# Kernel tuning notes

Measured on AMD Instinct MI355X. Metric: run time of the kernel, lower is better.

Reference implementation:

```python
import jax, jax.numpy as jnp
import numpy as np

N_NODES = 50000


def _gin_aggregate(x, src, dst):
    # sum_{j in N(i)} x_j via scatter-add over edges; eps=0 so add self term
    msg = x[src]  # [E, d]
    return x + jax.ops.segment_sum(msg, dst, num_segments=N_NODES)


def _mlp(h, Wa, ba, Wb, bb):
    return jax.nn.relu(h @ Wa + ba) @ Wb + bb


def setup_inputs() -> dict:
    key = jax.random.key(0)
    ks = jax.random.split(key, 12)
    d_in, d_h, n_cls, n_edges = 128, 128, 40, 800000
    x = jax.random.normal(ks[0], (N_NODES, d_in), dtype=jnp.float32)
    edge_index = jax.random.randint(ks[1], (2, n_edges), 0, N_NODES, dtype=jnp.int64)
    s = lambda k, sh: jax.random.normal(k, sh, dtype=jnp.float32) / np.sqrt(sh[0])
    return {
        "x": x,
        "edge_index": edge_index,
        "W11": s(ks[2], (d_in, 2 * d_h)), "b11": jnp.zeros((2 * d_h,), jnp.float32),
        "W12": s(ks[3], (2 * d_h, d_h)), "b12": jnp.zeros((d_h,), jnp.float32),
        "W21": s(ks[4], (d_h, 2 * d_h)), "b21": jnp.zeros((2 * d_h,), jnp.float32),
        "W22": s(ks[5], (2 * d_h, d_h)), "b22": jnp.zeros((d_h,), jnp.float32),
        "Wfc": s(ks[6], (d_h, n_cls)), "bfc": jnp.zeros((n_cls,), jnp.float32),
    }


def reference(x, edge_index, W11, b11, W12, b12, W21, b21, W22, b22, Wfc, bfc):
    src, dst = edge_index[0], edge_index[1]
    # GINConv 1: aggregate then MLP, followed by ReLU
    h = _mlp(_gin_aggregate(x, src, dst), W11, b11, W12, b12)
    h = jax.nn.relu(h)
    # GINConv 2
    h = _mlp(_gin_aggregate(h, src, dst), W21, b21, W22, b22)
    h = jax.nn.relu(h)
    # final classifier
    return h @ Wfc + bfc
```

## Files before the change

kernel.cpp:

```cpp
#include <hip/hip_runtime.h>

#define N_NODES 50000
#define N_EDGES 800000
#define NBUCK   392
#define EPB     2048
#define NSB     391
#define CAPB    2560

typedef __attribute__((ext_vector_type(8))) short short8;
typedef __attribute__((ext_vector_type(4))) float floatx4;

__device__ __forceinline__ float ubits(unsigned int b) {
    union { unsigned int i; float f; } v;
    v.i = b;
    return v.f;
}
__device__ __forceinline__ unsigned short f2b(float f) {
    union { float f; unsigned int i; } v;
    v.f = f;
    unsigned int r = v.i + 0x7FFFu + ((v.i >> 16) & 1u);
    return (unsigned short)(r >> 16);
}

__device__ __forceinline__ void pack_s1(const float* __restrict__ W,
                                        unsigned short* __restrict__ Wp,
                                        int blk, int tid) {
    int p = blk * 256 + tid;
    int j = p & 7, t2 = (p >> 3) & 255, v = p >> 11;
    int w = t2 >> 6, lane = t2 & 63, quad = lane >> 4, qm = lane & 15;
    int c = v >> 3, ks = (v >> 1) & 3, nt = v & 1;
    int k = ks * 32 + quad * 8 + j;
    int n = c * 128 + w * 32 + nt * 16 + qm;
    Wp[p] = f2b(W[k * 256 + n]);
}
__device__ __forceinline__ void pack_s2(const float* __restrict__ W,
                                        unsigned short* __restrict__ Wp,
                                        int blk, int tid) {
    int p = blk * 256 + tid;
    int j = p & 7, t2 = (p >> 3) & 255, v2 = p >> 11;
    int w = t2 >> 6, lane = t2 & 63, quad = lane >> 4, qm = lane & 15;
    int c2 = v2 >> 3, ks = v2 & 7;
    int k = ks * 32 + quad * 8 + j;
    int n = c2 * 32 + (w >> 1) * 16 + qm;
    Wp[p] = f2b(W[k * 128 + n]);
}

__global__ __launch_bounds__(256) void hist_conv(
    const int* __restrict__ dstv, const float* __restrict__ x,
    int* __restrict__ cnt, unsigned short* __restrict__ xb) {
    const int bid = blockIdx.x;
    const int tid = threadIdx.x;
    if (bid < NSB) {
        __shared__ int hist[NBUCK];
        const int k = bid;
        const int e0 = k * EPB;
        for (int i = tid; i < NBUCK; i += 256) hist[i] = 0;
        __syncthreads();
#pragma unroll
        for (int j = 0; j < EPB / 256; ++j) {
            int e = e0 + j * 256 + tid;
            if (e < N_EDGES) atomicAdd(&hist[dstv[e] >> 7], 1);
        }
        __syncthreads();
        for (int i = tid; i < NBUCK; i += 256) cnt[i * NSB + k] = hist[i];
    } else {
        int i = (bid - NSB) * 256 + tid;
        const float4 a = *reinterpret_cast<const float4*>(x + (size_t)i * 8);
        const float4 b = *reinterpret_cast<const float4*>(x + (size_t)i * 8 + 4);
        ushort4 u0, u1;
        u0.x = f2b(a.x); u0.y = f2b(a.y); u0.z = f2b(a.z); u0.w = f2b(a.w);
        u1.x = f2b(b.x); u1.y = f2b(b.y); u1.z = f2b(b.z); u1.w = f2b(b.w);
        *reinterpret_cast<ushort4*>(xb + (size_t)i * 8) = u0;
        *reinterpret_cast<ushort4*>(xb + (size_t)i * 8 + 4) = u1;
    }
}

__global__ __launch_bounds__(256) void scan_conv(
    const int* __restrict__ cnt, int* __restrict__ sbase,
    const float* __restrict__ W11, const float* __restrict__ W12,
    const float* __restrict__ W21, const float* __restrict__ W22,
    const float* __restrict__ Wfc,
    unsigned short* __restrict__ Wp11, unsigned short* __restrict__ Wp12,
    unsigned short* __restrict__ Wp21, unsigned short* __restrict__ Wp22,
    unsigned short* __restrict__ Wfct) {
    const int bid = blockIdx.x;
    const int tid = threadIdx.x;
    if (bid < NBUCK) {
        __shared__ int ps[256];
        __shared__ int sc[512];
        const int b = bid;
        sc[tid] = (tid < NSB) ? cnt[b * NSB + tid] : 0;
        sc[tid + 256] = (tid + 256 < NSB) ? cnt[b * NSB + tid + 256] : 0;
        __syncthreads();
        const int c0 = sc[2 * tid], c1 = sc[2 * tid + 1];
        ps[tid] = c0 + c1;
        __syncthreads();
        for (int off = 1; off < 256; off <<= 1) {
            int u = (tid >= off) ? ps[tid - off] : 0;
            __syncthreads();
            ps[tid] += u;
            __syncthreads();
        }
        if (tid < 196) {
            const int off0 = ps[tid] - (c0 + c1);
            sbase[b * 392 + 2 * tid] = off0;
            sbase[b * 392 + 2 * tid + 1] = off0 + c0;
        }
    } else if (bid < NBUCK + 128) {
        pack_s1(W11, Wp11, bid - NBUCK, tid);
    } else if (bid < NBUCK + 384) {
        pack_s2(W12, Wp12, bid - NBUCK - 128, tid);
    } else if (bid < NBUCK + 512) {
        pack_s1(W21, Wp21, bid - NBUCK - 384, tid);
    } else if (bid < NBUCK + 768) {
        pack_s2(W22, Wp22, bid - NBUCK - 512, tid);
    } else {
        int idx = (bid - NBUCK - 768) * 256 + tid;
        int n = idx >> 7, k = idx & 127;
        Wfct[idx] = (n < 40) ? f2b(Wfc[k * 40 + n]) : (unsigned short)0;
    }
}

__global__ __launch_bounds__(256) void place_compact(
    const int* __restrict__ srcv, const int* __restrict__ dstv,
    const int* __restrict__ sbase, int* __restrict__ bufc) {
    __shared__ int cur[NBUCK];
    const int k = blockIdx.x;
    const int tid = threadIdx.x;
    for (int i = tid; i < NBUCK; i += 256) cur[i] = sbase[i * 392 + k];
    __syncthreads();
    const int e0 = k * EPB;
#pragma unroll
    for (int j = 0; j < EPB / 256; ++j) {
        int e = e0 + j * 256 + tid;
        if (e < N_EDGES) {
            int d = dstv[e];
            int b = d >> 7;
            int pos = atomicAdd(&cur[b], 1);
            bufc[b * CAPB + pos] = srcv[e] | ((d & 127) << 16);
        }
    }
}

__global__ __launch_bounds__(256) void finish_buckets(
    const int* __restrict__ sbase, const int* __restrict__ bufc,
    int* __restrict__ e_src, int* __restrict__ row_ptr) {
    __shared__ int nc[128];
    __shared__ int ps[128];
    const int b = blockIdx.x;
    const int tid = threadIdx.x;
    const int S = sbase[b * 392 + 391];
    const int gb = b * CAPB;
    if (tid < 128) nc[tid] = 0;
    __syncthreads();
    for (int t = tid; t < S; t += 256)
        atomicAdd(&nc[(bufc[gb + t] >> 16) & 127], 1);
    __syncthreads();
    if (tid < 128) ps[tid] = nc[tid];
    __syncthreads();
    for (int off = 1; off < 128; off <<= 1) {
        int u = (tid >= off && tid < 128) ? ps[tid - off] : 0;
        __syncthreads();
        if (tid < 128) ps[tid] += u;
        __syncthreads();
    }
    if (tid < 128) {
        const int excl = ps[tid] - nc[tid];
        row_ptr[b * 129 + tid] = gb + excl;
        nc[tid] = gb + excl;
    }
    if (tid == 0) row_ptr[b * 129 + 128] = gb + S;
    __syncthreads();
    for (int t = tid; t < S; t += 256) {
        int p = bufc[gb + t];
        int pos = atomicAdd(&nc[(p >> 16) & 127], 1);
        e_src[pos] = p & 0xFFFF;
    }
}

__global__ __launch_bounds__(256) void agg_bf16q(const unsigned short* __restrict__ X,
                                                 const int* __restrict__ row_ptr,
                                                 const int* __restrict__ e_src,
                                                 unsigned short* __restrict__ agg) {
    const int node = (blockIdx.x * 256 + threadIdx.x) >> 6;
    const int lane = threadIdx.x & 63;
    const int qw = lane >> 4, ql = lane & 15;
    const size_t off = (size_t)ql * 8;

    const int rp = node + (node >> 7);
    const int beg = row_ptr[rp], end = row_ptr[rp + 1];
    float acc[8];
#pragma unroll
    for (int k = 0; k < 8; ++k) acc[k] = 0.f;

    if (qw == 0) {
        uint4 u = *reinterpret_cast<const uint4*>(X + (size_t)node * 128 + off);
        const unsigned int* up = (const unsigned int*)&u;
#pragma unroll
        for (int k = 0; k < 4; ++k) {
            acc[2 * k]     += ubits(up[k] << 16);
            acc[2 * k + 1] += ubits(up[k] & 0xFFFF0000u);
        }
    }

    int e = beg + qw;
    for (; e + 12 < end; e += 16) {
        const int s0 = e_src[e], s1 = e_src[e + 4], s2 = e_src[e + 8], s3 = e_src[e + 12];
        uint4 u0 = *reinterpret_cast<const uint4*>(X + (size_t)s0 * 128 + off);
        uint4 u1 = *reinterpret_cast<const uint4*>(X + (size_t)s1 * 128 + off);
        uint4 u2 = *reinterpret_cast<const uint4*>(X + (size_t)s2 * 128 + off);
        uint4 u3 = *reinterpret_cast<const uint4*>(X + (size_t)s3 * 128 + off);
        const unsigned int* p0 = (const unsigned int*)&u0;
        const unsigned int* p1 = (const unsigned int*)&u1;
        const unsigned int* p2 = (const unsigned int*)&u2;
        const unsigned int* p3 = (const unsigned int*)&u3;
#pragma unroll
        for (int k = 0; k < 4; ++k) {
            acc[2 * k]     += ubits(p0[k] << 16) + ubits(p1[k] << 16)
                            + ubits(p2[k] << 16) + ubits(p3[k] << 16);
            acc[2 * k + 1] += ubits(p0[k] & 0xFFFF0000u) + ubits(p1[k] & 0xFFFF0000u)
                            + ubits(p2[k] & 0xFFFF0000u) + ubits(p3[k] & 0xFFFF0000u);
        }
    }
    for (; e + 4 < end; e += 8) {
        const int s0 = e_src[e], s1 = e_src[e + 4];
        uint4 u0 = *reinterpret_cast<const uint4*>(X + (size_t)s0 * 128 + off);
        uint4 u1 = *reinterpret_cast<const uint4*>(X + (size_t)s1 * 128 + off);
        const unsigned int* p0 = (const unsigned int*)&u0;
        const unsigned int* p1 = (const unsigned int*)&u1;
#pragma unroll
        for (int k = 0; k < 4; ++k) {
            acc[2 * k]     += ubits(p0[k] << 16) + ubits(p1[k] << 16);
            acc[2 * k + 1] += ubits(p0[k] & 0xFFFF0000u) + ubits(p1[k] & 0xFFFF0000u);
        }
    }
    if (e < end) {
        const int s = e_src[e];
        uint4 u = *reinterpret_cast<const uint4*>(X + (size_t)s * 128 + off);
        const unsigned int* p = (const unsigned int*)&u;
#pragma unroll
        for (int k = 0; k < 4; ++k) {
            acc[2 * k]     += ubits(p[k] << 16);
            acc[2 * k + 1] += ubits(p[k] & 0xFFFF0000u);
        }
    }

#pragma unroll
    for (int k = 0; k < 8; ++k) acc[k] += __shfl_xor(acc[k], 32);
#pragma unroll
    for (int k = 0; k < 8; ++k) acc[k] += __shfl_xor(acc[k], 16);

    if (qw == 0) {
        ushort4 o0, o1;
        o0.x = f2b(acc[0]); o0.y = f2b(acc[1]); o0.z = f2b(acc[2]); o0.w = f2b(acc[3]);
        o1.x = f2b(acc[4]); o1.y = f2b(acc[5]); o1.z = f2b(acc[6]); o1.w = f2b(acc[7]);
        unsigned short* p = agg + (size_t)node * 128 + off;
        *reinterpret_cast<ushort4*>(p) = o0;
        *reinterpret_cast<ushort4*>(p + 4) = o1;
    }
}

template <bool FUSE>
__global__ __launch_bounds__(256, 2) void mlp_fused(
    const unsigned short* __restrict__ X, const unsigned short* __restrict__ Wp1,
    const float* __restrict__ b1, const unsigned short* __restrict__ Wp2,
    const float* __restrict__ b2, unsigned short* __restrict__ Y,
    const unsigned short* __restrict__ Wfct, const float* __restrict__ bfc,
    float* __restrict__ out, int M) {
    __shared__ __align__(16) char smem[FUSE ? 68608 : 51200];
    unsigned short* A  = (unsigned short*)smem;
    unsigned short* T  = (unsigned short*)(smem + 17408);
    unsigned short* Hf = (unsigned short*)(smem + 51200);

    const int tid = threadIdx.x;
    const int m0 = blockIdx.x * 64;
    const int lane = tid & 63, w = tid >> 6;
    const int qm = lane & 15, quad = lane >> 4;

    short8 wb1[16];
#pragma unroll
    for (int v = 0; v < 16; ++v)
        wb1[v] = *reinterpret_cast<const short8*>(Wp1 + ((v * 256 + tid) << 3));

#pragma unroll
    for (int j = 0; j < 4; ++j) {
        int i = j * 256 + tid;
        int r = i >> 4, c8 = (i & 15) << 3;
        uint4 v = {0, 0, 0, 0};
        if (m0 + r < M) v = *reinterpret_cast<const uint4*>(X + (size_t)(m0 + r) * 128 + c8);
        *reinterpret_cast<uint4*>(&A[r * 136 + c8]) = v;
    }
    __syncthreads();

#pragma unroll
    for (int c = 0; c < 2; ++c) {
        floatx4 acc1[4][2];
#pragma unroll
        for (int mt = 0; mt < 4; ++mt)
#pragma unroll
            for (int nt = 0; nt < 2; ++nt) acc1[mt][nt] = {0.f, 0.f, 0.f, 0.f};
#pragma unroll
        for (int ks = 0; ks < 4; ++ks) {
            const int kb = ks * 32 + quad * 8;
            short8 a[4];
#pragma unroll
            for (int mt = 0; mt < 4; ++mt)
                a[mt] = *reinterpret_cast<const short8*>(&A[(mt * 16 + qm) * 136 + kb]);
#pragma unroll
            for (int mt = 0; mt < 4; ++mt)
#pragma unroll
                for (int nt = 0; nt < 2; ++nt)
                    acc1[mt][nt] = __builtin_amdgcn_mfma_f32_16x16x32_bf16(
                        a[mt], wb1[c * 8 + ks * 2 + nt], acc1[mt][nt], 0, 0, 0);
        }
#pragma unroll
        for (int nt = 0; nt < 2; ++nt) {
            const int jcol = c * 128 + w * 32 + nt * 16 + qm;
            const float bj = b1[jcol];
#pragma unroll
            for (int mt = 0; mt < 4; ++mt)
#pragma unroll
                for (int r = 0; r < 4; ++r)
                    T[(mt * 16 + quad * 4 + r) * 264 + jcol] =
                        f2b(fmaxf(acc1[mt][nt][r] + bj, 0.f));
        }
    }

    short8 wb2[32];
#pragma unroll
    for (int v = 0; v < 32; ++v)
        wb2[v] = *reinterpret_cast<const short8*>(Wp2 + ((v * 256 + tid) << 3));
    __syncthreads();

#pragma unroll
    for (int c2 = 0; c2 < 4; ++c2) {
        floatx4 acc2[2];
        acc2[0] = {0.f, 0.f, 0.f, 0.f};
        acc2[1] = {0.f, 0.f, 0.f, 0.f};
#pragma unroll
        for (int ks = 0; ks < 8; ++ks) {
            const int kb = ks * 32 + quad * 8;
            short8 t0 = *reinterpret_cast<const short8*>(&T[((w & 1) * 32 + qm) * 264 + kb]);
            short8 t1 = *reinterpret_cast<const short8*>(&T[((w & 1) * 32 + 16 + qm) * 264 + kb]);
            acc2[0] = __builtin_amdgcn_mfma_f32_16x16x32_bf16(t0, wb2[c2 * 8 + ks], acc2[0], 0, 0, 0);
            acc2[1] = __builtin_amdgcn_mfma_f32_16x16x32_bf16(t1, wb2[c2 * 8 + ks], acc2[1], 0, 0, 0);
        }

        const int ncol = c2 * 32 + (w >> 1) * 16 + qm;
        const float bj = b2[ncol];
        if (!FUSE) {
#pragma unroll
            for (int mt2 = 0; mt2 < 2; ++mt2)
#pragma unroll
                for (int r = 0; r < 4; ++r) {
                    int row = m0 + (w & 1) * 32 + mt2 * 16 + quad * 4 + r;
                    if (row < M)
                        Y[(size_t)row * 128 + ncol] = f2b(fmaxf(acc2[mt2][r] + bj, 0.f));
                }
        } else {
#pragma unroll
            for (int mt2 = 0; mt2 < 2; ++mt2)
#pragma unroll
                for (int r = 0; r < 4; ++r)
                    Hf[((w & 1) * 32 + mt2 * 16 + quad * 4 + r) * 136 + ncol] =
                        f2b(fmaxf(acc2[mt2][r] + bj, 0.f));
        }
    }

    if (FUSE) {
        __syncthreads();
        floatx4 cacc[3];
#pragma unroll
        for (int nt = 0; nt < 3; ++nt) cacc[nt] = {0.f, 0.f, 0.f, 0.f};
#pragma unroll
        for (int c2 = 0; c2 < 4; ++c2) {
            short8 hf = *reinterpret_cast<const short8*>(
                &Hf[(w * 16 + qm) * 136 + c2 * 32 + quad * 8]);
#pragma unroll
            for (int nt = 0; nt < 3; ++nt) {
                short8 bf = *reinterpret_cast<const short8*>(
                    Wfct + (nt * 16 + qm) * 128 + c2 * 32 + quad * 8);
                cacc[nt] = __builtin_amdgcn_mfma_f32_16x16x32_bf16(hf, bf, cacc[nt], 0, 0, 0);
            }
        }
#pragma unroll
        for (int nt = 0; nt < 3; ++nt) {
            int col = nt * 16 + qm;
            if (col < 40) {
                const float bj = bfc[col];
#pragma unroll
                for (int r = 0; r < 4; ++r) {
                    int row = m0 + w * 16 + quad * 4 + r;
                    if (row < M) out[(size_t)row * 40 + col] = cacc[nt][r] + bj;
                }
            }
        }
    }
}

extern "C" void kernel_launch(void* const* d_in, const int* in_sizes, int n_in,
                              void* d_out, int out_size, void* d_ws, size_t ws_size,
                              hipStream_t stream) {
    const float* x   = (const float*)d_in[0];
    const int*   ei  = (const int*)d_in[1];
    const float* W11 = (const float*)d_in[2];
    const float* b11 = (const float*)d_in[3];
    const float* W12 = (const float*)d_in[4];
    const float* b12 = (const float*)d_in[5];
    const float* W21 = (const float*)d_in[6];
    const float* b21 = (const float*)d_in[7];
    const float* W22 = (const float*)d_in[8];
    const float* b22 = (const float*)d_in[9];
    const float* Wfc = (const float*)d_in[10];
    const float* bfc = (const float*)d_in[11];
    float* out = (float*)d_out;

    const int* srcv = ei;
    const int* dstv = ei + N_EDGES;

    unsigned short* agg  = (unsigned short*)d_ws;
    unsigned short* h    = agg + (size_t)N_NODES * 128;
    unsigned short* xb   = h   + (size_t)N_NODES * 128;
    unsigned short* Wp11 = xb  + (size_t)N_NODES * 128;
    unsigned short* Wp12 = Wp11 + 32768;
    unsigned short* Wp21 = Wp12 + 65536;
    unsigned short* Wp22 = Wp21 + 32768;
    unsigned short* Wfct = Wp22 + 65536;
    int* cnt     = (int*)(Wfct + 48 * 128);
    int* sbase   = cnt + 153664;
    int* row_ptr = sbase + 153664;
    int* e_src   = row_ptr + 50688;
    int* bufc    = e_src + (size_t)NBUCK * CAPB;

    hist_conv<<<NSB + 3125, 256, 0, stream>>>(dstv, x, cnt, xb);

    scan_conv<<<NBUCK + 792, 256, 0, stream>>>(
        cnt, sbase, W11, W12, W21, W22, Wfc,
        Wp11, Wp12, Wp21, Wp22, Wfct);

    place_compact<<<NSB, 256, 0, stream>>>(srcv, dstv, sbase, bufc);

    finish_buckets<<<NBUCK, 256, 0, stream>>>(sbase, bufc, e_src, row_ptr);

    const int agg_blocks = N_NODES * 64 / 256;
    const int mlp_blocks = (N_NODES + 63) / 64;

    agg_bf16q<<<agg_blocks, 256, 0, stream>>>(xb, row_ptr, e_src, agg);
    mlp_fused<false><<<mlp_blocks, 256, 0, stream>>>(
        agg, Wp11, b11, Wp12, b12, h, nullptr, nullptr, nullptr, N_NODES);
    agg_bf16q<<<agg_blocks, 256, 0, stream>>>(h, row_ptr, e_src, agg);
    mlp_fused<true><<<mlp_blocks, 256, 0, stream>>>(
        agg, Wp21, b21, Wp22, b22, nullptr, Wfct, bfc, out, N_NODES);
}
```

Before: 226.1 us.

## Replace histogram-scan-place pipeline with global atomic bucket reservation

The separate histogram, per-bucket scan and placement kernels are merged into one scatter kernel. Each block reserves its slots in every bucket with a global atomicAdd on a per-bucket counter, then writes edges into them. The per-bucket CSR finish now runs inside the weight-conversion kernel. This drops two launches and the large count and base arrays, at the cost of a memset, global atomic contention, and edge order within a bucket that varies from run to run (float summation order may change).

Result: no change. 223.8 us (-1.0%).

```diff
diff --git a/kernel.cpp b/kernel.cpp
--- a/kernel.cpp
+++ b/kernel.cpp
@@ -45,24 +45,44 @@
     Wp[p] = f2b(W[k * 128 + n]);
 }
 
-__global__ __launch_bounds__(256) void hist_conv(
-    const int* __restrict__ dstv, const float* __restrict__ x,
-    int* __restrict__ cnt, unsigned short* __restrict__ xb) {
+__global__ __launch_bounds__(256) void scatter_all(
+    const int* __restrict__ srcv, const int* __restrict__ dstv,
+    const float* __restrict__ x,
+    int* __restrict__ bcount, int* __restrict__ bufc,
+    unsigned short* __restrict__ xb) {
     const int bid = blockIdx.x;
     const int tid = threadIdx.x;
     if (bid < NSB) {
         __shared__ int hist[NBUCK];
-        const int k = bid;
-        const int e0 = k * EPB;
+        __shared__ int base[NBUCK];
+        const int e0 = bid * EPB;
+        int d[8], s[8];
+#pragma unroll
+        for (int j = 0; j < 8; ++j) {
+            int e = e0 + j * 256 + tid;
+            if (e < N_EDGES) { d[j] = dstv[e]; s[j] = srcv[e]; }
+            else d[j] = -1;
+        }
         for (int i = tid; i < NBUCK; i += 256) hist[i] = 0;
         __syncthreads();
 #pragma unroll
-        for (int j = 0; j < EPB / 256; ++j) {
-            int e = e0 + j * 256 + tid;
-            if (e < N_EDGES) atomicAdd(&hist[dstv[e] >> 7], 1);
-        }
-        __syncthreads();
-        for (int i = tid; i < NBUCK; i += 256) cnt[i * NSB + k] = hist[i];
+        for (int j = 0; j < 8; ++j)
+            if (d[j] >= 0) atomicAdd(&hist[d[j] >> 7], 1);
+        __syncthreads();
+        for (int i = tid; i < NBUCK; i += 256) {
+            int c = hist[i];
+            base[i] = c ? atomicAdd(&bcount[i], c) : 0;
+            hist[i] = 0;
+        }
+        __syncthreads();
+#pragma unroll
+        for (int j = 0; j < 8; ++j) {
+            if (d[j] >= 0) {
+                int b = d[j] >> 7;
+                int r = atomicAdd(&hist[b], 1);
+                bufc[b * CAPB + base[b] + r] = s[j] | ((d[j] & 127) << 16);
+            }
+        }
     } else {
         int i = (bid - NSB) * 256 + tid;
         const float4 a = *reinterpret_cast<const float4*>(x + (size_t)i * 8);
@@ -75,8 +95,9 @@
     }
 }
 
-__global__ __launch_bounds__(256) void scan_conv(
-    const int* __restrict__ cnt, int* __restrict__ sbase,
+__global__ __launch_bounds__(256) void finish_conv(
+    const int* __restrict__ bcount, const int* __restrict__ bufc,
+    int* __restrict__ e_src, int* __restrict__ row_ptr,
     const float* __restrict__ W11, const float* __restrict__ W12,
     const float* __restrict__ W21, const float* __restrict__ W22,
     const float* __restrict__ Wfc,
@@ -86,25 +107,35 @@
     const int bid = blockIdx.x;
     const int tid = threadIdx.x;
     if (bid < NBUCK) {
-        __shared__ int ps[256];
-        __shared__ int sc[512];
+        __shared__ int nc[128];
+        __shared__ int ps[128];
         const int b = bid;
-        sc[tid] = (tid < NSB) ? cnt[b * NSB + tid] : 0;
-        sc[tid + 256] = (tid + 256 < NSB) ? cnt[b * NSB + tid + 256] : 0;
-        __syncthreads();
-        const int c0 = sc[2 * tid], c1 = sc[2 * tid + 1];
-        ps[tid] = c0 + c1;
-        __syncthreads();
-        for (int off = 1; off < 256; off <<= 1) {
-            int u = (tid >= off) ? ps[tid - off] : 0;
+        const int S = bcount[b];
+        const int gb = b * CAPB;
+        if (tid < 128) nc[tid] = 0;
+        __syncthreads();
+        for (int t = tid; t < S; t += 256)
+            atomicAdd(&nc[(bufc[gb + t] >> 16) & 127], 1);
+        __syncthreads();
+        if (tid < 128) ps[tid] = nc[tid];
+        __syncthreads();
+        for (int off = 1; off < 128; off <<= 1) {
+            int u = (tid >= off && tid < 128) ? ps[tid - off] : 0;
             __syncthreads();
-            ps[tid] += u;
+            if (tid < 128) ps[tid] += u;
             __syncthreads();
         }
-        if (tid < 196) {
-            const int off0 = ps[tid] - (c0 + c1);
-            sbase[b * 392 + 2 * tid] = off0;
-            sbase[b * 392 + 2 * tid + 1] = off0 + c0;
+        if (tid < 128) {
+            const int excl = ps[tid] - nc[tid];
+            row_ptr[b * 129 + tid] = gb + excl;
+            nc[tid] = gb + excl;
+        }
+        if (tid == 0) row_ptr[b * 129 + 128] = gb + S;
+        __syncthreads();
+        for (int t = tid; t < S; t += 256) {
+            int p = bufc[gb + t];
+            int pos = atomicAdd(&nc[(p >> 16) & 127], 1);
+            e_src[pos] = p & 0xFFFF;
         }
     } else if (bid < NBUCK + 128) {
         pack_s1(W11, Wp11, bid - NBUCK, tid);
@@ -118,63 +149,6 @@
         int idx = (bid - NBUCK - 768) * 256 + tid;
         int n = idx >> 7, k = idx & 127;
         Wfct[idx] = (n < 40) ? f2b(Wfc[k * 40 + n]) : (unsigned short)0;
-    }
-}
-
-__global__ __launch_bounds__(256) void place_compact(
-    const int* __restrict__ srcv, const int* __restrict__ dstv,
-    const int* __restrict__ sbase, int* __restrict__ bufc) {
-    __shared__ int cur[NBUCK];
-    const int k = blockIdx.x;
-    const int tid = threadIdx.x;
-    for (int i = tid; i < NBUCK; i += 256) cur[i] = sbase[i * 392 + k];
-    __syncthreads();
-    const int e0 = k * EPB;
-#pragma unroll
-    for (int j = 0; j < EPB / 256; ++j) {
-        int e = e0 + j * 256 + tid;
-        if (e < N_EDGES) {
-            int d = dstv[e];
-            int b = d >> 7;
-            int pos = atomicAdd(&cur[b], 1);
-            bufc[b * CAPB + pos] = srcv[e] | ((d & 127) << 16);
-        }
-    }
-}
-
-__global__ __launch_bounds__(256) void finish_buckets(
-    const int* __restrict__ sbase, const int* __restrict__ bufc,
-    int* __restrict__ e_src, int* __restrict__ row_ptr) {
-    __shared__ int nc[128];
-    __shared__ int ps[128];
-    const int b = blockIdx.x;
-    const int tid = threadIdx.x;
-    const int S = sbase[b * 392 + 391];
-    const int gb = b * CAPB;
-    if (tid < 128) nc[tid] = 0;
-    __syncthreads();
-    for (int t = tid; t < S; t += 256)
-        atomicAdd(&nc[(bufc[gb + t] >> 16) & 127], 1);
-    __syncthreads();
-    if (tid < 128) ps[tid] = nc[tid];
-    __syncthreads();
-    for (int off = 1; off < 128; off <<= 1) {
-        int u = (tid >= off && tid < 128) ? ps[tid - off] : 0;
-        __syncthreads();
-        if (tid < 128) ps[tid] += u;
-        __syncthreads();
-    }
-    if (tid < 128) {
-        const int excl = ps[tid] - nc[tid];
-        row_ptr[b * 129 + tid] = gb + excl;
-        nc[tid] = gb + excl;
-    }
-    if (tid == 0) row_ptr[b * 129 + 128] = gb + S;
-    __syncthreads();
-    for (int t = tid; t < S; t += 256) {
-        int p = bufc[gb + t];
-        int pos = atomicAdd(&nc[(p >> 16) & 127], 1);
-        e_src[pos] = p & 0xFFFF;
     }
 }
 
@@ -426,21 +400,19 @@
     unsigned short* Wp21 = Wp12 + 65536;
     unsigned short* Wp22 = Wp21 + 32768;
     unsigned short* Wfct = Wp22 + 65536;
-    int* cnt     = (int*)(Wfct + 48 * 128);
-    int* sbase   = cnt + 153664;
-    int* row_ptr = sbase + 153664;
+    int* bcount  = (int*)(Wfct + 48 * 128);
+    int* row_ptr = bcount + 512;
     int* e_src   = row_ptr + 50688;
     int* bufc    = e_src + (size_t)NBUCK * CAPB;
 
-    hist_conv<<<NSB + 3125, 256, 0, stream>>>(dstv, x, cnt, xb);
-
-    scan_conv<<<NBUCK + 792, 256, 0, stream>>>(
-        cnt, sbase, W11, W12, W21, W22, Wfc,
+    hipMemsetAsync(bcount, 0, NBUCK * sizeof(int), stream);
+
+    scatter_all<<<NSB + 3125, 256, 0, stream>>>(srcv, dstv, x, bcount, bufc, xb);
+
+    finish_conv<<<NBUCK + 792, 256, 0, stream>>>(
+        bcount, bufc, e_src, row_ptr,
+        W11, W12, W21, W22, Wfc,
         Wp11, Wp12, Wp21, Wp22, Wfct);
-
-    place_compact<<<NSB, 256, 0, stream>>>(srcv, dstv, sbase, bufc);
-
-    finish_buckets<<<NBUCK, 256, 0, stream>>>(sbase, bufc, e_src, row_ptr);
 
     const int agg_blocks = N_NODES * 64 / 256;
     const int mlp_blocks = (N_NODES + 63) / 64;
```
